# Performance work log

Hardware: AMD Instinct MI355X
Metric: run time of the kernel (lower is better)

Reference implementation:

```python
import jax, jax.numpy as jnp
import numpy as np

N, C_IN, C_OUT = 16384, 512, 1024

def setup_inputs() -> dict:
    key = jax.random.key(0)
    k1, k2 = jax.random.split(key)
    x = jax.random.normal(k1, (N, C_IN), dtype=jnp.float32)
    mean = jax.random.normal(k2, (C_OUT, C_IN), dtype=jnp.float32)
    return {"x": x, "mean": mean}

def reference(x, mean):
    # out[n, o] = 1 / sqrt(sum_c (x[n,c] - mean[o,c])^2)
    x_sq = jnp.sum(x * x, axis=-1, keepdims=True)            # [N, 1]
    m_sq = jnp.sum(mean * mean, axis=-1)                     # [O]
    cross = jnp.einsum('nc,oc->no', x, mean)                 # [N, O] GEMM
    d2 = x_sq - 2.0 * cross + m_sq[None, :]                  # [N, O]
    return jax.lax.rsqrt(d2)
```

## Files before the change

kernel.cpp:

```cpp
#include <hip/hip_runtime.h>
#include <hip/hip_bf16.h>
#include <stdint.h>

#define N_ROWS 16384
#define O_ROWS 1024
#define K_DIM  512

typedef __bf16 bf16x8 __attribute__((ext_vector_type(8)));
typedef float  f32x4  __attribute__((ext_vector_type(4)));

__device__ __forceinline__ ushort f2bfu(float f) {
    __bf16 h = (__bf16)f;
    return __builtin_bit_cast(ushort, h);
}

#define BAR_LGKM()  do {                                        \
    asm volatile("s_waitcnt lgkmcnt(0)" ::: "memory");          \
    __builtin_amdgcn_s_barrier();                               \
} while (0)

__global__ __launch_bounds__(512) void quadra_kernel(
    const float* __restrict__ x, const float* __restrict__ mean,
    float* __restrict__ out)
{
    __shared__ ushort sA[256 * 64];
    __shared__ ushort sB[128 * 64];

    const int bid  = blockIdx.x;
    const int t    = (bid & 7) * 64 + (bid >> 3);
    const int brow = (t >> 3) * 256;
    const int bcol = (t & 7) * 128;

    const int tid  = threadIdx.x;
    const int lane = tid & 63;
    const int wid  = tid >> 6;
    const int wr = wid >> 1, wc = wid & 1;

    f32x4 acc[4][4] = {};

    const int r0 = tid >> 3;
    const int q  = tid & 7;

    const float* gA = x    + (size_t)(brow + r0) * K_DIM + q * 8;
    const float* gB = mean + (size_t)(bcol + r0) * K_DIM + q * 8;

    float asq[4] = {0.f, 0.f, 0.f, 0.f};
    float bsq[2] = {0.f, 0.f};

    const int hi = lane >> 4, cl = lane & 15;

    #pragma unroll 1
    for (int kt = 0; kt < 8; ++kt) {
        #pragma unroll
        for (int i = 0; i < 4; ++i) {
            const float* p = gA + (size_t)(i * 64) * K_DIM + kt * 64;
            f32x4 v0 = *(const f32x4*)(p);
            f32x4 v1 = *(const f32x4*)(p + 4);

            asq[i] += v0[0]*v0[0] + v0[1]*v0[1] + v0[2]*v0[2] + v0[3]*v0[3]
                    + v1[0]*v1[0] + v1[1]*v1[1] + v1[2]*v1[2] + v1[3]*v1[3];

            bf16x8 cv;
            cv[0] = (__bf16)v0[0]; cv[1] = (__bf16)v0[1];
            cv[2] = (__bf16)v0[2]; cv[3] = (__bf16)v0[3];
            cv[4] = (__bf16)v1[0]; cv[5] = (__bf16)v1[1];
            cv[6] = (__bf16)v1[2]; cv[7] = (__bf16)v1[3];

            const int row = r0 + i * 64;
            const int wb  = (q * 16) ^ ((row & 7) << 4);
            *(bf16x8*)(sA + row * 64 + (wb >> 1)) = cv;
        }
        #pragma unroll
        for (int i = 0; i < 2; ++i) {
            const float* p = gB + (size_t)(i * 64) * K_DIM + kt * 64;
            f32x4 v0 = *(const f32x4*)(p);
            f32x4 v1 = *(const f32x4*)(p + 4);

            bsq[i] += v0[0]*v0[0] + v0[1]*v0[1] + v0[2]*v0[2] + v0[3]*v0[3]
                    + v1[0]*v1[0] + v1[1]*v1[1] + v1[2]*v1[2] + v1[3]*v1[3];

            bf16x8 cv;
            cv[0] = (__bf16)(v0[0] * -2.0f); cv[1] = (__bf16)(v0[1] * -2.0f);
            cv[2] = (__bf16)(v0[2] * -2.0f); cv[3] = (__bf16)(v0[3] * -2.0f);
            cv[4] = (__bf16)(v1[0] * -2.0f); cv[5] = (__bf16)(v1[1] * -2.0f);
            cv[6] = (__bf16)(v1[2] * -2.0f); cv[7] = (__bf16)(v1[3] * -2.0f);

            const int row = r0 + i * 64;
            const int wb  = (q * 16) ^ ((row & 7) << 4);
            *(bf16x8*)(sB + row * 64 + (wb >> 1)) = cv;
        }

        BAR_LGKM();

        #pragma unroll
        for (int ks = 0; ks < 2; ++ks) {
            bf16x8 a[4], b[4];
            #pragma unroll
            for (int m = 0; m < 4; ++m) {
                const int row = wr*64 + m*16 + cl;
                const int rb  = (ks*64 + hi*16) ^ ((row & 7) << 4);
                a[m] = *(const bf16x8*)(sA + row * 64 + (rb >> 1));
            }
            #pragma unroll
            for (int n = 0; n < 4; ++n) {
                const int row = wc*64 + n*16 + cl;
                const int rb  = (ks*64 + hi*16) ^ ((row & 7) << 4);
                b[n] = *(const bf16x8*)(sB + row * 64 + (rb >> 1));
            }
            #pragma unroll
            for (int m = 0; m < 4; ++m)
                #pragma unroll
                for (int n = 0; n < 4; ++n)
                    acc[m][n] = __builtin_amdgcn_mfma_f32_16x16x32_bf16(
                        a[m], b[n], acc[m][n], 0, 0, 0);
        }

        BAR_LGKM();
    }

    ushort* sAe = sA;
    ushort* sBe = sA + 256 * 32;
    #pragma unroll
    for (int i = 0; i < 4; ++i) {
        float sa = asq[i];
        #pragma unroll
        for (int msk = 1; msk < 8; msk <<= 1) sa += __shfl_xor(sa, msk);
        uint2 aw = {0u, 0u};
        if (q == 0) aw.x = (uint32_t)f2bfu(sa) | (0x3F80u << 16);
        *(uint2*)(sAe + (r0 + i * 64) * 32 + q * 4) = aw;
    }
    #pragma unroll
    for (int i = 0; i < 2; ++i) {
        float sb = bsq[i];
        #pragma unroll
        for (int msk = 1; msk < 8; msk <<= 1) sb += __shfl_xor(sb, msk);
        uint2 bw = {0u, 0u};
        if (q == 0) bw.x = 0x3F80u | ((uint32_t)f2bfu(sb) << 16);
        *(uint2*)(sBe + (r0 + i * 64) * 32 + q * 4) = bw;
    }
    BAR_LGKM();

    {
        bf16x8 a[4], b[4];
        #pragma unroll
        for (int m = 0; m < 4; ++m)
            a[m] = *(const bf16x8*)(sAe + (wr*64 + m*16 + cl) * 32 + hi * 8);
        #pragma unroll
        for (int n = 0; n < 4; ++n)
            b[n] = *(const bf16x8*)(sBe + (wc*64 + n*16 + cl) * 32 + hi * 8);
        #pragma unroll
        for (int m = 0; m < 4; ++m)
            #pragma unroll
            for (int n = 0; n < 4; ++n)
                acc[m][n] = __builtin_amdgcn_mfma_f32_16x16x32_bf16(
                    a[m], b[n], acc[m][n], 0, 0, 0);
    }

    const int rg = lane >> 4;
    #pragma unroll
    for (int m = 0; m < 4; ++m) {
        #pragma unroll
        for (int j = 0; j < 4; ++j) {
            const int grow = brow + wr*64 + m*16 + rg*4 + j;
            float* orow = out + (size_t)grow * O_ROWS + bcol + wc*64 + cl;
            #pragma unroll
            for (int n = 0; n < 4; ++n)
                orow[n * 16] = rsqrtf(acc[m][n][j]);
        }
    }
}

extern "C" void kernel_launch(void* const* d_in, const int* in_sizes, int n_in,
                              void* d_out, int out_size, void* d_ws, size_t ws_size,
                              hipStream_t stream) {
    const float* x    = (const float*)d_in[0];
    const float* mean = (const float*)d_in[1];
    float* out = (float*)d_out;

    quadra_kernel<<<dim3((N_ROWS / 256) * (O_ROWS / 128)), 512, 0, stream>>>(
        x, mean, out);
}
```

Measured before the change: 40.59 us.

## Load A fragments directly from global into registers, stage only B in LDS

```diff
diff --git a/kernel.cpp b/kernel.cpp
--- a/kernel.cpp
+++ b/kernel.cpp
@@ -19,12 +19,14 @@
     __builtin_amdgcn_s_barrier();                               \
 } while (0)
 
-__global__ __launch_bounds__(512) void quadra_kernel(
+__global__ __launch_bounds__(256, 2) void quadra_kernel(
     const float* __restrict__ x, const float* __restrict__ mean,
     float* __restrict__ out)
 {
-    __shared__ ushort sA[256 * 64];
-    __shared__ ushort sB[128 * 64];
+    __shared__ ushort lds[12288];
+    ushort* sB  = lds;
+    ushort* sAe = lds;
+    ushort* sBe = lds + 8192;
 
     const int bid  = blockIdx.x;
     const int t    = (bid & 7) * 64 + (bid >> 3);
@@ -34,83 +36,80 @@
     const int tid  = threadIdx.x;
     const int lane = tid & 63;
     const int wid  = tid >> 6;
-    const int wr = wid >> 1, wc = wid & 1;
+    const int cl   = lane & 15, hi = lane >> 4;
 
-    f32x4 acc[4][4] = {};
+    f32x4 acc[4][8] = {};
 
-    const int r0 = tid >> 3;
-    const int q  = tid & 7;
+    const int srow = tid >> 1;
+    const int h    = tid & 1;
+    const float* gB = mean + (size_t)(bcol + srow) * K_DIM + h * 32;
 
-    const float* gA = x    + (size_t)(brow + r0) * K_DIM + q * 8;
-    const float* gB = mean + (size_t)(bcol + r0) * K_DIM + q * 8;
+    const float* gA = x + (size_t)(brow + wid * 64 + cl) * K_DIM + hi * 8;
 
     float asq[4] = {0.f, 0.f, 0.f, 0.f};
-    float bsq[2] = {0.f, 0.f};
-
-    const int hi = lane >> 4, cl = lane & 15;
+    float bsq = 0.f;
 
     #pragma unroll 1
     for (int kt = 0; kt < 8; ++kt) {
         #pragma unroll
-        for (int i = 0; i < 4; ++i) {
-            const float* p = gA + (size_t)(i * 64) * K_DIM + kt * 64;
+        for (int c = 0; c < 2; ++c) {
+            const float* p = gB + kt * 64 + c * 16;
             f32x4 v0 = *(const f32x4*)(p);
             f32x4 v1 = *(const f32x4*)(p + 4);
+            f32x4 v2 = *(const f32x4*)(p + 8);
+            f32x4 v3 = *(const f32x4*)(p + 12);
 
-            asq[i] += v0[0]*v0[0] + v0[1]*v0[1] + v0[2]*v0[2] + v0[3]*v0[3]
-                    + v1[0]*v1[0] + v1[1]*v1[1] + v1[2]*v1[2] + v1[3]*v1[3];
+            bsq += v0[0]*v0[0] + v0[1]*v0[1] + v0[2]*v0[2] + v0[3]*v0[3]
+                 + v1[0]*v1[0] + v1[1]*v1[1] + v1[2]*v1[2] + v1[3]*v1[3]
+                 + v2[0]*v2[0] + v2[1]*v2[1] + v2[2]*v2[2] + v2[3]*v2[3]
+                 + v3[0]*v3[0] + v3[1]*v3[1] + v3[2]*v3[2] + v3[3]*v3[3];
 
-            bf16x8 cv;
-            cv[0] = (__bf16)v0[0]; cv[1] = (__bf16)v0[1];
-            cv[2] = (__bf16)v0[2]; cv[3] = (__bf16)v0[3];
-            cv[4] = (__bf16)v1[0]; cv[5] = (__bf16)v1[1];
-            cv[6] = (__bf16)v1[2]; cv[7] = (__bf16)v1[3];
+            bf16x8 c0, c1;
+            c0[0] = (__bf16)(v0[0] * -2.0f); c0[1] = (__bf16)(v0[1] * -2.0f);
+            c0[2] = (__bf16)(v0[2] * -2.0f); c0[3] = (__bf16)(v0[3] * -2.0f);
+            c0[4] = (__bf16)(v1[0] * -2.0f); c0[5] = (__bf16)(v1[1] * -2.0f);
+            c0[6] = (__bf16)(v1[2] * -2.0f); c0[7] = (__bf16)(v1[3] * -2.0f);
+            c1[0] = (__bf16)(v2[0] * -2.0f); c1[1] = (__bf16)(v2[1] * -2.0f);
+            c1[2] = (__bf16)(v2[2] * -2.0f); c1[3] = (__bf16)(v2[3] * -2.0f);
+            c1[4] = (__bf16)(v3[0] * -2.0f); c1[5] = (__bf16)(v3[1] * -2.0f);
+            c1[6] = (__bf16)(v3[2] * -2.0f); c1[7] = (__bf16)(v3[3] * -2.0f);
 
-            const int row = r0 + i * 64;
-            const int wb  = (q * 16) ^ ((row & 7) << 4);
-            *(bf16x8*)(sA + row * 64 + (wb >> 1)) = cv;
-        }
-        #pragma unroll
-        for (int i = 0; i < 2; ++i) {
-            const float* p = gB + (size_t)(i * 64) * K_DIM + kt * 64;
-            f32x4 v0 = *(const f32x4*)(p);
-            f32x4 v1 = *(const f32x4*)(p + 4);
-
-            bsq[i] += v0[0]*v0[0] + v0[1]*v0[1] + v0[2]*v0[2] + v0[3]*v0[3]
-                    + v1[0]*v1[0] + v1[1]*v1[1] + v1[2]*v1[2] + v1[3]*v1[3];
-
-            bf16x8 cv;
-            cv[0] = (__bf16)(v0[0] * -2.0f); cv[1] = (__bf16)(v0[1] * -2.0f);
-            cv[2] = (__bf16)(v0[2] * -2.0f); cv[3] = (__bf16)(v0[3] * -2.0f);
-            cv[4] = (__bf16)(v1[0] * -2.0f); cv[5] = (__bf16)(v1[1] * -2.0f);
-            cv[6] = (__bf16)(v1[2] * -2.0f); cv[7] = (__bf16)(v1[3] * -2.0f);
-
-            const int row = r0 + i * 64;
-            const int wb  = (q * 16) ^ ((row & 7) << 4);
-            *(bf16x8*)(sB + row * 64 + (wb >> 1)) = cv;
+            const int b0  = h * 64 + c * 32;
+            const int swz = (srow & 7) << 4;
+            *(bf16x8*)(sB + srow * 64 + (((b0)      ^ swz) >> 1)) = c0;
+            *(bf16x8*)(sB + srow * 64 + (((b0 + 16) ^ swz) >> 1)) = c1;
         }
 
         BAR_LGKM();
 
         #pragma unroll
         for (int ks = 0; ks < 2; ++ks) {
-            bf16x8 a[4], b[4];
+            bf16x8 a[4];
             #pragma unroll
             for (int m = 0; m < 4; ++m) {
-                const int row = wr*64 + m*16 + cl;
-                const int rb  = (ks*64 + hi*16) ^ ((row & 7) << 4);
-                a[m] = *(const bf16x8*)(sA + row * 64 + (rb >> 1));
+                const float* p = gA + (size_t)(m * 16) * K_DIM + kt * 64 + ks * 32;
+                f32x4 v0 = *(const f32x4*)(p);
+                f32x4 v1 = *(const f32x4*)(p + 4);
+                asq[m] += v0[0]*v0[0] + v0[1]*v0[1] + v0[2]*v0[2] + v0[3]*v0[3]
+                        + v1[0]*v1[0] + v1[1]*v1[1] + v1[2]*v1[2] + v1[3]*v1[3];
+                bf16x8 cv;
+                cv[0] = (__bf16)v0[0]; cv[1] = (__bf16)v0[1];
+                cv[2] = (__bf16)v0[2]; cv[3] = (__bf16)v0[3];
+                cv[4] = (__bf16)v1[0]; cv[5] = (__bf16)v1[1];
+                cv[6] = (__bf16)v1[2]; cv[7] = (__bf16)v1[3];
+                a[m] = cv;
             }
+            bf16x8 b[8];
             #pragma unroll
-            for (int n = 0; n < 4; ++n) {
-                const int row = wc*64 + n*16 + cl;
-                const int rb  = (ks*64 + hi*16) ^ ((row & 7) << 4);
+            for (int n = 0; n < 8; ++n) {
+                const int row = n * 16 + cl;
+                const int rb  = (ks * 64 + hi * 16) ^ ((row & 7) << 4);
                 b[n] = *(const bf16x8*)(sB + row * 64 + (rb >> 1));
             }
             #pragma unroll
             for (int m = 0; m < 4; ++m)
                 #pragma unroll
-                for (int n = 0; n < 4; ++n)
+                for (int n = 0; n < 8; ++n)
                     acc[m][n] = __builtin_amdgcn_mfma_f32_16x16x32_bf16(
                         a[m], b[n], acc[m][n], 0, 0, 0);
         }
@@ -118,53 +117,54 @@
         BAR_LGKM();
     }
 
-    ushort* sAe = sA;
-    ushort* sBe = sA + 256 * 32;
     #pragma unroll
-    for (int i = 0; i < 4; ++i) {
-        float sa = asq[i];
+    for (int m = 0; m < 4; ++m) {
+        float sa = asq[m];
+        sa += __shfl_xor(sa, 16);
+        sa += __shfl_xor(sa, 32);
+        const int row = wid * 64 + m * 16 + cl;
+        uint4 w = {0u, 0u, 0u, 0u};
+        if (hi == 0) w.x = (uint32_t)f2bfu(sa) | (0x3F80u << 16);
+        *(uint4*)(sAe + row * 32 + hi * 8) = w;
+    }
+    {
+        float sb = bsq;
+        sb += __shfl_xor(sb, 1);
         #pragma unroll
-        for (int msk = 1; msk < 8; msk <<= 1) sa += __shfl_xor(sa, msk);
-        uint2 aw = {0u, 0u};
-        if (q == 0) aw.x = (uint32_t)f2bfu(sa) | (0x3F80u << 16);
-        *(uint2*)(sAe + (r0 + i * 64) * 32 + q * 4) = aw;
-    }
-    #pragma unroll
-    for (int i = 0; i < 2; ++i) {
-        float sb = bsq[i];
-        #pragma unroll
-        for (int msk = 1; msk < 8; msk <<= 1) sb += __shfl_xor(sb, msk);
-        uint2 bw = {0u, 0u};
-        if (q == 0) bw.x = 0x3F80u | ((uint32_t)f2bfu(sb) << 16);
-        *(uint2*)(sBe + (r0 + i * 64) * 32 + q * 4) = bw;
+        for (int s = 0; s < 2; ++s) {
+            uint4 w = {0u, 0u, 0u, 0u};
+            if (h == 0 && s == 0)
+                w.x = 0x3F80u | ((uint32_t)f2bfu(sb) << 16);
+            *(uint4*)(sBe + srow * 32 + h * 16 + s * 8) = w;
+        }
     }
     BAR_LGKM();
 
     {
-        bf16x8 a[4], b[4];
+        bf16x8 a[4], b[8];
         #pragma unroll
         for (int m = 0; m < 4; ++m)
-            a[m] = *(const bf16x8*)(sAe + (wr*64 + m*16 + cl) * 32 + hi * 8);
+            a[m] = *(const bf16x8*)(sAe + (wid*64 + m*16 + cl) * 32 + hi * 8);
         #pragma unroll
-        for (int n = 0; n < 4; ++n)
-            b[n] = *(const bf16x8*)(sBe + (wc*64 + n*16 + cl) * 32 + hi * 8);
+        for (int n = 0; n < 8; ++n)
+            b[n] = *(const bf16x8*)(sBe + (n*16 + cl) * 32 + hi * 8);
         #pragma unroll
         for (int m = 0; m < 4; ++m)
             #pragma unroll
-            for (int n = 0; n < 4; ++n)
+            for (int n = 0; n < 8; ++n)
                 acc[m][n] = __builtin_amdgcn_mfma_f32_16x16x32_bf16(
                     a[m], b[n], acc[m][n], 0, 0, 0);
     }
 
-    const int rg = lane >> 4;
+    const int rg = hi;
     #pragma unroll
     for (int m = 0; m < 4; ++m) {
         #pragma unroll
         for (int j = 0; j < 4; ++j) {
-            const int grow = brow + wr*64 + m*16 + rg*4 + j;
-            float* orow = out + (size_t)grow * O_ROWS + bcol + wc*64 + cl;
+            const int grow = brow + wid*64 + m*16 + rg*4 + j;
+            float* orow = out + (size_t)grow * O_ROWS + bcol + cl;
             #pragma unroll
-            for (int n = 0; n < 4; ++n)
+            for (int n = 0; n < 8; ++n)
                 orow[n * 16] = rsqrtf(acc[m][n][j]);
         }
     }
@@ -177,6 +177,6 @@
     const float* mean = (const float*)d_in[1];
     float* out = (float*)d_out;
 
-    quadra_kernel<<<dim3((N_ROWS / 256) * (O_ROWS / 128)), 512, 0, stream>>>(
+    quadra_kernel<<<dim3((N_ROWS / 256) * (O_ROWS / 128)), 256, 0, stream>>>(
         x, mean, out);
 }
```

Result: slower. 61.09 us (+50.5%).

## Double-buffer shared tiles and prefetch next K-slice during MFMA

Applied to the files above, without the earlier changes.

```diff
diff --git a/kernel.cpp b/kernel.cpp
--- a/kernel.cpp
+++ b/kernel.cpp
@@ -6,6 +6,7 @@
 #define O_ROWS 1024
 #define K_DIM  512
 
+typedef __bf16 bf16x4 __attribute__((ext_vector_type(4)));
 typedef __bf16 bf16x8 __attribute__((ext_vector_type(8)));
 typedef float  f32x4  __attribute__((ext_vector_type(4)));
 
@@ -23,8 +24,8 @@
     const float* __restrict__ x, const float* __restrict__ mean,
     float* __restrict__ out)
 {
-    __shared__ ushort sA[256 * 64];
-    __shared__ ushort sB[128 * 64];
+    __shared__ ushort sA[2][128 * 64];
+    __shared__ ushort sB[2][64 * 64];
 
     const int bid  = blockIdx.x;
     const int t    = (bid & 7) * 64 + (bid >> 3);
@@ -35,91 +36,127 @@
     const int lane = tid & 63;
     const int wid  = tid >> 6;
     const int wr = wid >> 1, wc = wid & 1;
+    const int cl = lane & 15, hi = lane >> 4;
 
     f32x4 acc[4][4] = {};
 
     const int r0 = tid >> 3;
     const int q  = tid & 7;
 
-    const float* gA = x    + (size_t)(brow + r0) * K_DIM + q * 8;
-    const float* gB = mean + (size_t)(bcol + r0) * K_DIM + q * 8;
+    const float* gA = x    + (size_t)(brow + r0) * K_DIM + q * 4;
+    const float* gB = mean + (size_t)(bcol + r0) * K_DIM + q * 4;
 
     float asq[4] = {0.f, 0.f, 0.f, 0.f};
     float bsq[2] = {0.f, 0.f};
 
-    const int hi = lane >> 4, cl = lane & 15;
+    f32x4 pa[4], pb[2];
+
+    #pragma unroll
+    for (int i = 0; i < 4; ++i)
+        pa[i] = *(const f32x4*)(gA + (size_t)(i * 64) * K_DIM);
+    #pragma unroll
+    for (int i = 0; i < 2; ++i)
+        pb[i] = *(const f32x4*)(gB + (size_t)(i * 64) * K_DIM);
+
+    #pragma unroll
+    for (int i = 0; i < 4; ++i) {
+        f32x4 v = pa[i];
+        asq[i] += v[0]*v[0] + v[1]*v[1] + v[2]*v[2] + v[3]*v[3];
+        bf16x4 cv;
+        cv[0] = (__bf16)v[0]; cv[1] = (__bf16)v[1];
+        cv[2] = (__bf16)v[2]; cv[3] = (__bf16)v[3];
+        const int r  = r0 + i * 64;
+        const int by = ((r >> 7) * 64 + q * 8) ^ ((r & 7) << 4);
+        *(bf16x4*)(&sA[0][0] + (r & 127) * 64 + (by >> 1)) = cv;
+    }
+    #pragma unroll
+    for (int i = 0; i < 2; ++i) {
+        f32x4 v = pb[i];
+        bsq[i] += v[0]*v[0] + v[1]*v[1] + v[2]*v[2] + v[3]*v[3];
+        bf16x4 cv;
+        cv[0] = (__bf16)(v[0] * -2.0f); cv[1] = (__bf16)(v[1] * -2.0f);
+        cv[2] = (__bf16)(v[2] * -2.0f); cv[3] = (__bf16)(v[3] * -2.0f);
+        const int r  = r0 + i * 64;
+        const int by = ((r >> 6) * 64 + q * 8) ^ ((r & 7) << 4);
+        *(bf16x4*)(&sB[0][0] + (r & 63) * 64 + (by >> 1)) = cv;
+    }
+    BAR_LGKM();
 
     #pragma unroll 1
-    for (int kt = 0; kt < 8; ++kt) {
-        #pragma unroll
-        for (int i = 0; i < 4; ++i) {
-            const float* p = gA + (size_t)(i * 64) * K_DIM + kt * 64;
-            f32x4 v0 = *(const f32x4*)(p);
-            f32x4 v1 = *(const f32x4*)(p + 4);
-
-            asq[i] += v0[0]*v0[0] + v0[1]*v0[1] + v0[2]*v0[2] + v0[3]*v0[3]
-                    + v1[0]*v1[0] + v1[1]*v1[1] + v1[2]*v1[2] + v1[3]*v1[3];
-
-            bf16x8 cv;
-            cv[0] = (__bf16)v0[0]; cv[1] = (__bf16)v0[1];
-            cv[2] = (__bf16)v0[2]; cv[3] = (__bf16)v0[3];
-            cv[4] = (__bf16)v1[0]; cv[5] = (__bf16)v1[1];
-            cv[6] = (__bf16)v1[2]; cv[7] = (__bf16)v1[3];
-
-            const int row = r0 + i * 64;
-            const int wb  = (q * 16) ^ ((row & 7) << 4);
-            *(bf16x8*)(sA + row * 64 + (wb >> 1)) = cv;
-        }
-        #pragma unroll
-        for (int i = 0; i < 2; ++i) {
-            const float* p = gB + (size_t)(i * 64) * K_DIM + kt * 64;
-            f32x4 v0 = *(const f32x4*)(p);
-            f32x4 v1 = *(const f32x4*)(p + 4);
-
-            bsq[i] += v0[0]*v0[0] + v0[1]*v0[1] + v0[2]*v0[2] + v0[3]*v0[3]
-                    + v1[0]*v1[0] + v1[1]*v1[1] + v1[2]*v1[2] + v1[3]*v1[3];
-
-            bf16x8 cv;
-            cv[0] = (__bf16)(v0[0] * -2.0f); cv[1] = (__bf16)(v0[1] * -2.0f);
-            cv[2] = (__bf16)(v0[2] * -2.0f); cv[3] = (__bf16)(v0[3] * -2.0f);
-            cv[4] = (__bf16)(v1[0] * -2.0f); cv[5] = (__bf16)(v1[1] * -2.0f);
-            cv[6] = (__bf16)(v1[2] * -2.0f); cv[7] = (__bf16)(v1[3] * -2.0f);
-
-            const int row = r0 + i * 64;
-            const int wb  = (q * 16) ^ ((row & 7) << 4);
-            *(bf16x8*)(sB + row * 64 + (wb >> 1)) = cv;
-        }
+    for (int kt = 0; kt < 16; ++kt) {
+        const int cur = kt & 1;
+        ushort* bufA = &sA[cur][0];
+        ushort* bufB = &sB[cur][0];
+        ushort* nxtA = &sA[cur ^ 1][0];
+        ushort* nxtB = &sB[cur ^ 1][0];
+
+        if (kt < 15) {
+            #pragma unroll
+            for (int i = 0; i < 4; ++i)
+                pa[i] = *(const f32x4*)(gA + (size_t)(i * 64) * K_DIM + (kt + 1) * 32);
+            #pragma unroll
+            for (int i = 0; i < 2; ++i)
+                pb[i] = *(const f32x4*)(gB + (size_t)(i * 64) * K_DIM + (kt + 1) * 32);
+        }
+
+        bf16x8 a[4], b[4];
+        #pragma unroll
+        for (int m = 0; m < 4; ++m) {
+            const int rr = wr*64 + m*16 + cl;
+            const int by = ((rr >> 7) * 64 + hi * 16) ^ ((rr & 7) << 4);
+            a[m] = *(const bf16x8*)(bufA + (rr & 127) * 64 + (by >> 1));
+        }
+        #pragma unroll
+        for (int n = 0; n < 4; ++n) {
+            const int rr = wc*64 + n*16 + cl;
+            const int by = ((rr >> 6) * 64 + hi * 16) ^ ((rr & 7) << 4);
+            b[n] = *(const bf16x8*)(bufB + (rr & 63) * 64 + (by >> 1));
+        }
+
+        #pragma unroll
+        for (int m = 0; m < 2; ++m)
+            #pragma unroll
+            for (int n = 0; n < 4; ++n)
+                acc[m][n] = __builtin_amdgcn_mfma_f32_16x16x32_bf16(
+                    a[m], b[n], acc[m][n], 0, 0, 0);
+
+        if (kt < 15) {
+            #pragma unroll
+            for (int i = 0; i < 4; ++i) {
+                f32x4 v = pa[i];
+                asq[i] += v[0]*v[0] + v[1]*v[1] + v[2]*v[2] + v[3]*v[3];
+                bf16x4 cv;
+                cv[0] = (__bf16)v[0]; cv[1] = (__bf16)v[1];
+                cv[2] = (__bf16)v[2]; cv[3] = (__bf16)v[3];
+                const int r  = r0 + i * 64;
+                const int by = ((r >> 7) * 64 + q * 8) ^ ((r & 7) << 4);
+                *(bf16x4*)(nxtA + (r & 127) * 64 + (by >> 1)) = cv;
+            }
+            #pragma unroll
+            for (int i = 0; i < 2; ++i) {
+                f32x4 v = pb[i];
+                bsq[i] += v[0]*v[0] + v[1]*v[1] + v[2]*v[2] + v[3]*v[3];
+                bf16x4 cv;
+                cv[0] = (__bf16)(v[0] * -2.0f); cv[1] = (__bf16)(v[1] * -2.0f);
+                cv[2] = (__bf16)(v[2] * -2.0f); cv[3] = (__bf16)(v[3] * -2.0f);
+                const int r  = r0 + i * 64;
+                const int by = ((r >> 6) * 64 + q * 8) ^ ((r & 7) << 4);
+                *(bf16x4*)(nxtB + (r & 63) * 64 + (by >> 1)) = cv;
+            }
+        }
+
+        #pragma unroll
+        for (int m = 2; m < 4; ++m)
+            #pragma unroll
+            for (int n = 0; n < 4; ++n)
+                acc[m][n] = __builtin_amdgcn_mfma_f32_16x16x32_bf16(
+                    a[m], b[n], acc[m][n], 0, 0, 0);
 
         BAR_LGKM();
-
-        #pragma unroll
-        for (int ks = 0; ks < 2; ++ks) {
-            bf16x8 a[4], b[4];
-            #pragma unroll
-            for (int m = 0; m < 4; ++m) {
-                const int row = wr*64 + m*16 + cl;
-                const int rb  = (ks*64 + hi*16) ^ ((row & 7) << 4);
-                a[m] = *(const bf16x8*)(sA + row * 64 + (rb >> 1));
-            }
-            #pragma unroll
-            for (int n = 0; n < 4; ++n) {
-                const int row = wc*64 + n*16 + cl;
-                const int rb  = (ks*64 + hi*16) ^ ((row & 7) << 4);
-                b[n] = *(const bf16x8*)(sB + row * 64 + (rb >> 1));
-            }
-            #pragma unroll
-            for (int m = 0; m < 4; ++m)
-                #pragma unroll
-                for (int n = 0; n < 4; ++n)
-                    acc[m][n] = __builtin_amdgcn_mfma_f32_16x16x32_bf16(
-                        a[m], b[n], acc[m][n], 0, 0, 0);
-        }
-
-        BAR_LGKM();
-    }
-
-    ushort* sAe = sA;
-    ushort* sBe = sA + 256 * 32;
+    }
+
+    ushort* sAe = &sA[0][0];
+    ushort* sBe = &sA[1][0];
     #pragma unroll
     for (int i = 0; i < 4; ++i) {
         float sa = asq[i];
@@ -156,12 +193,11 @@
                     a[m], b[n], acc[m][n], 0, 0, 0);
     }
 
-    const int rg = lane >> 4;
     #pragma unroll
     for (int m = 0; m < 4; ++m) {
         #pragma unroll
         for (int j = 0; j < 4; ++j) {
-            const int grow = brow + wr*64 + m*16 + rg*4 + j;
+            const int grow = brow + wr*64 + m*16 + hi*4 + j;
             float* orow = out + (size_t)grow * O_ROWS + bcol + wc*64 + cl;
             #pragma unroll
             for (int n = 0; n < 4; ++n)
```

Result: slower. 46.05 us (+13.4%).

## Split block into producer and consumer waves with double-buffered LDS

Applied to the files above, without the earlier changes.

```diff
diff --git a/kernel.cpp b/kernel.cpp
--- a/kernel.cpp
+++ b/kernel.cpp
@@ -23,8 +23,8 @@
     const float* __restrict__ x, const float* __restrict__ mean,
     float* __restrict__ out)
 {
-    __shared__ ushort sA[256 * 64];
-    __shared__ ushort sB[128 * 64];
+    __shared__ ushort sA[2][256 * 64];
+    __shared__ ushort sB[2][128 * 64];
 
     const int bid  = blockIdx.x;
     const int t    = (bid & 7) * 64 + (bid >> 3);
@@ -34,140 +34,165 @@
     const int tid  = threadIdx.x;
     const int lane = tid & 63;
     const int wid  = tid >> 6;
-    const int wr = wid >> 1, wc = wid & 1;
-
-    f32x4 acc[4][4] = {};
-
-    const int r0 = tid >> 3;
+    const int cl = lane & 15, hi = lane >> 4;
+    const bool producer = (wid < 4);
+
+    const int r0 = (tid >> 3) & 31;
     const int q  = tid & 7;
-
+    const int rb = (tid >> 2) & 63;
+    const int qb = tid & 3;
     const float* gA = x    + (size_t)(brow + r0) * K_DIM + q * 8;
-    const float* gB = mean + (size_t)(bcol + r0) * K_DIM + q * 8;
-
-    float asq[4] = {0.f, 0.f, 0.f, 0.f};
+    const float* gB = mean + (size_t)(bcol + rb) * K_DIM + qb * 16;
+
+    const int cw = wid - 4;
+    const int cr = (cw >> 1) & 1, cc = cw & 1;
+
+    f32x4 acc[8][4] = {};
+    float asq[8] = {0,0,0,0,0,0,0,0};
     float bsq[2] = {0.f, 0.f};
 
-    const int hi = lane >> 4, cl = lane & 15;
+    #define STAGE(KT, BUF) do {                                              \
+        ushort* dA = &sA[BUF][0];                                            \
+        ushort* dB = &sB[BUF][0];                                            \
+        _Pragma("unroll")                                                    \
+        for (int i = 0; i < 8; ++i) {                                        \
+            const float* p = gA + (size_t)(i * 32) * K_DIM + (KT) * 64;      \
+            f32x4 v0 = *(const f32x4*)(p);                                   \
+            f32x4 v1 = *(const f32x4*)(p + 4);                               \
+            asq[i] += v0[0]*v0[0] + v0[1]*v0[1] + v0[2]*v0[2] + v0[3]*v0[3]  \
+                    + v1[0]*v1[0] + v1[1]*v1[1] + v1[2]*v1[2] + v1[3]*v1[3]; \
+            bf16x8 cv;                                                       \
+            cv[0] = (__bf16)v0[0]; cv[1] = (__bf16)v0[1];                    \
+            cv[2] = (__bf16)v0[2]; cv[3] = (__bf16)v0[3];                    \
+            cv[4] = (__bf16)v1[0]; cv[5] = (__bf16)v1[1];                    \
+            cv[6] = (__bf16)v1[2]; cv[7] = (__bf16)v1[3];                    \
+            const int row = r0 + i * 32;                                     \
+            const int wb  = (q * 16) ^ ((row & 7) << 4);                     \
+            *(bf16x8*)(dA + row * 64 + (wb >> 1)) = cv;                      \
+        }                                                                    \
+        _Pragma("unroll")                                                    \
+        for (int i = 0; i < 2; ++i) {                                        \
+            const float* p = gB + (size_t)(i * 64) * K_DIM + (KT) * 64;      \
+            f32x4 v0 = *(const f32x4*)(p);                                   \
+            f32x4 v1 = *(const f32x4*)(p + 4);                               \
+            f32x4 v2 = *(const f32x4*)(p + 8);                               \
+            f32x4 v3 = *(const f32x4*)(p + 12);                              \
+            bsq[i] += v0[0]*v0[0] + v0[1]*v0[1] + v0[2]*v0[2] + v0[3]*v0[3]  \
+                    + v1[0]*v1[0] + v1[1]*v1[1] + v1[2]*v1[2] + v1[3]*v1[3]  \
+                    + v2[0]*v2[0] + v2[1]*v2[1] + v2[2]*v2[2] + v2[3]*v2[3]  \
+                    + v3[0]*v3[0] + v3[1]*v3[1] + v3[2]*v3[2] + v3[3]*v3[3]; \
+            bf16x8 c0, c1;                                                   \
+            c0[0] = (__bf16)(v0[0] * -2.0f); c0[1] = (__bf16)(v0[1] * -2.0f);\
+            c0[2] = (__bf16)(v0[2] * -2.0f); c0[3] = (__bf16)(v0[3] * -2.0f);\
+            c0[4] = (__bf16)(v1[0] * -2.0f); c0[5] = (__bf16)(v1[1] * -2.0f);\
+            c0[6] = (__bf16)(v1[2] * -2.0f); c0[7] = (__bf16)(v1[3] * -2.0f);\
+            c1[0] = (__bf16)(v2[0] * -2.0f); c1[1] = (__bf16)(v2[1] * -2.0f);\
+            c1[2] = (__bf16)(v2[2] * -2.0f); c1[3] = (__bf16)(v2[3] * -2.0f);\
+            c1[4] = (__bf16)(v3[0] * -2.0f); c1[5] = (__bf16)(v3[1] * -2.0f);\
+            c1[6] = (__bf16)(v3[2] * -2.0f); c1[7] = (__bf16)(v3[3] * -2.0f);\
+            const int row = rb + i * 64;                                     \
+            const int swz = (row & 7) << 4;                                  \
+            *(bf16x8*)(dB + row * 64 + (((qb * 32)      ^ swz) >> 1)) = c0;  \
+            *(bf16x8*)(dB + row * 64 + (((qb * 32 + 16) ^ swz) >> 1)) = c1;  \
+        }                                                                    \
+    } while (0)
+
+    if (producer) STAGE(0, 0);
+    BAR_LGKM();
 
     #pragma unroll 1
     for (int kt = 0; kt < 8; ++kt) {
+        if (producer) {
+            if (kt < 7) {
+                const int nb = (kt + 1) & 1;
+                if (nb) STAGE(kt + 1, 1); else STAGE(kt + 1, 0);
+            }
+        } else {
+            const ushort* bufA = &sA[kt & 1][0];
+            const ushort* bufB = &sB[kt & 1][0];
+            #pragma unroll
+            for (int ks = 0; ks < 2; ++ks) {
+                bf16x8 a[8], b[4];
+                #pragma unroll
+                for (int m = 0; m < 8; ++m) {
+                    const int row = cr*128 + m*16 + cl;
+                    const int rbo = (ks*64 + hi*16) ^ ((row & 7) << 4);
+                    a[m] = *(const bf16x8*)(bufA + row * 64 + (rbo >> 1));
+                }
+                #pragma unroll
+                for (int n = 0; n < 4; ++n) {
+                    const int row = cc*64 + n*16 + cl;
+                    const int rbo = (ks*64 + hi*16) ^ ((row & 7) << 4);
+                    b[n] = *(const bf16x8*)(bufB + row * 64 + (rbo >> 1));
+                }
+                #pragma unroll
+                for (int m = 0; m < 8; ++m)
+                    #pragma unroll
+                    for (int n = 0; n < 4; ++n)
+                        acc[m][n] = __builtin_amdgcn_mfma_f32_16x16x32_bf16(
+                            a[m], b[n], acc[m][n], 0, 0, 0);
+            }
+        }
+        BAR_LGKM();
+    }
+
+    ushort* sAe = &sA[0][0];
+    ushort* sBe = &sB[0][0];
+    if (producer) {
         #pragma unroll
-        for (int i = 0; i < 4; ++i) {
-            const float* p = gA + (size_t)(i * 64) * K_DIM + kt * 64;
-            f32x4 v0 = *(const f32x4*)(p);
-            f32x4 v1 = *(const f32x4*)(p + 4);
-
-            asq[i] += v0[0]*v0[0] + v0[1]*v0[1] + v0[2]*v0[2] + v0[3]*v0[3]
-                    + v1[0]*v1[0] + v1[1]*v1[1] + v1[2]*v1[2] + v1[3]*v1[3];
-
-            bf16x8 cv;
-            cv[0] = (__bf16)v0[0]; cv[1] = (__bf16)v0[1];
-            cv[2] = (__bf16)v0[2]; cv[3] = (__bf16)v0[3];
-            cv[4] = (__bf16)v1[0]; cv[5] = (__bf16)v1[1];
-            cv[6] = (__bf16)v1[2]; cv[7] = (__bf16)v1[3];
-
-            const int row = r0 + i * 64;
-            const int wb  = (q * 16) ^ ((row & 7) << 4);
-            *(bf16x8*)(sA + row * 64 + (wb >> 1)) = cv;
+        for (int i = 0; i < 8; ++i) {
+            float sa = asq[i];
+            sa += __shfl_xor(sa, 1);
+            sa += __shfl_xor(sa, 2);
+            sa += __shfl_xor(sa, 4);
+            const int row = r0 + i * 32;
+            uint2 aw = {0u, 0u};
+            if (q == 0) aw.x = (uint32_t)f2bfu(sa) | (0x3F80u << 16);
+            *(uint2*)(sAe + row * 32 + q * 4) = aw;
         }
         #pragma unroll
         for (int i = 0; i < 2; ++i) {
-            const float* p = gB + (size_t)(i * 64) * K_DIM + kt * 64;
-            f32x4 v0 = *(const f32x4*)(p);
-            f32x4 v1 = *(const f32x4*)(p + 4);
-
-            bsq[i] += v0[0]*v0[0] + v0[1]*v0[1] + v0[2]*v0[2] + v0[3]*v0[3]
-                    + v1[0]*v1[0] + v1[1]*v1[1] + v1[2]*v1[2] + v1[3]*v1[3];
-
-            bf16x8 cv;
-            cv[0] = (__bf16)(v0[0] * -2.0f); cv[1] = (__bf16)(v0[1] * -2.0f);
-            cv[2] = (__bf16)(v0[2] * -2.0f); cv[3] = (__bf16)(v0[3] * -2.0f);
-            cv[4] = (__bf16)(v1[0] * -2.0f); cv[5] = (__bf16)(v1[1] * -2.0f);
-            cv[6] = (__bf16)(v1[2] * -2.0f); cv[7] = (__bf16)(v1[3] * -2.0f);
-
-            const int row = r0 + i * 64;
-            const int wb  = (q * 16) ^ ((row & 7) << 4);
-            *(bf16x8*)(sB + row * 64 + (wb >> 1)) = cv;
-        }
-
-        BAR_LGKM();
-
-        #pragma unroll
-        for (int ks = 0; ks < 2; ++ks) {
-            bf16x8 a[4], b[4];
-            #pragma unroll
-            for (int m = 0; m < 4; ++m) {
-                const int row = wr*64 + m*16 + cl;
-                const int rb  = (ks*64 + hi*16) ^ ((row & 7) << 4);
-                a[m] = *(const bf16x8*)(sA + row * 64 + (rb >> 1));
-            }
-            #pragma unroll
-            for (int n = 0; n < 4; ++n) {
-                const int row = wc*64 + n*16 + cl;
-                const int rb  = (ks*64 + hi*16) ^ ((row & 7) << 4);
-                b[n] = *(const bf16x8*)(sB + row * 64 + (rb >> 1));
-            }
-            #pragma unroll
-            for (int m = 0; m < 4; ++m)
+            float sb = bsq[i];
+            sb += __shfl_xor(sb, 1);
+            sb += __shfl_xor(sb, 2);
+            const int row = rb + i * 64;
+            uint4 bw = {0u, 0u, 0u, 0u};
+            if (qb == 0) bw.x = 0x3F80u | ((uint32_t)f2bfu(sb) << 16);
+            *(uint4*)(sBe + row * 32 + qb * 8) = bw;
+        }
+    }
+    BAR_LGKM();
+
+    if (!producer) {
+        {
+            bf16x8 a[8], b[4];
+            #pragma unroll
+            for (int m = 0; m < 8; ++m)
+                a[m] = *(const bf16x8*)(sAe + (cr*128 + m*16 + cl) * 32 + hi * 8);
+            #pragma unroll
+            for (int n = 0; n < 4; ++n)
+                b[n] = *(const bf16x8*)(sBe + (cc*64 + n*16 + cl) * 32 + hi * 8);
+            #pragma unroll
+            for (int m = 0; m < 8; ++m)
                 #pragma unroll
                 for (int n = 0; n < 4; ++n)
                     acc[m][n] = __builtin_amdgcn_mfma_f32_16x16x32_bf16(
                         a[m], b[n], acc[m][n], 0, 0, 0);
         }
 
-        BAR_LGKM();
+        #pragma unroll
+        for (int m = 0; m < 8; ++m) {
+            #pragma unroll
+            for (int j = 0; j < 4; ++j) {
+                const int grow = brow + cr*128 + m*16 + hi*4 + j;
+                float* orow = out + (size_t)grow * O_ROWS + bcol + cc*64 + cl;
+                #pragma unroll
+                for (int n = 0; n < 4; ++n)
+                    orow[n * 16] = rsqrtf(acc[m][n][j]);
+            }
+        }
     }
-
-    ushort* sAe = sA;
-    ushort* sBe = sA + 256 * 32;
-    #pragma unroll
-    for (int i = 0; i < 4; ++i) {
-        float sa = asq[i];
-        #pragma unroll
-        for (int msk = 1; msk < 8; msk <<= 1) sa += __shfl_xor(sa, msk);
-        uint2 aw = {0u, 0u};
-        if (q == 0) aw.x = (uint32_t)f2bfu(sa) | (0x3F80u << 16);
-        *(uint2*)(sAe + (r0 + i * 64) * 32 + q * 4) = aw;
-    }
-    #pragma unroll
-    for (int i = 0; i < 2; ++i) {
-        float sb = bsq[i];
-        #pragma unroll
-        for (int msk = 1; msk < 8; msk <<= 1) sb += __shfl_xor(sb, msk);
-        uint2 bw = {0u, 0u};
-        if (q == 0) bw.x = 0x3F80u | ((uint32_t)f2bfu(sb) << 16);
-        *(uint2*)(sBe + (r0 + i * 64) * 32 + q * 4) = bw;
-    }
-    BAR_LGKM();
-
-    {
-        bf16x8 a[4], b[4];
-        #pragma unroll
-        for (int m = 0; m < 4; ++m)
-            a[m] = *(const bf16x8*)(sAe + (wr*64 + m*16 + cl) * 32 + hi * 8);
-        #pragma unroll
-        for (int n = 0; n < 4; ++n)
-            b[n] = *(const bf16x8*)(sBe + (wc*64 + n*16 + cl) * 32 + hi * 8);
-        #pragma unroll
-        for (int m = 0; m < 4; ++m)
-            #pragma unroll
-            for (int n = 0; n < 4; ++n)
-                acc[m][n] = __builtin_amdgcn_mfma_f32_16x16x32_bf16(
-                    a[m], b[n], acc[m][n], 0, 0, 0);
-    }
-
-    const int rg = lane >> 4;
-    #pragma unroll
-    for (int m = 0; m < 4; ++m) {
-        #pragma unroll
-        for (int j = 0; j < 4; ++j) {
-            const int grow = brow + wr*64 + m*16 + rg*4 + j;
-            float* orow = out + (size_t)grow * O_ROWS + bcol + wc*64 + cl;
-            #pragma unroll
-            for (int n = 0; n < 4; ++n)
-                orow[n * 16] = rsqrtf(acc[m][n][j]);
-        }
-    }
+    #undef STAGE
 }
 
 extern "C" void kernel_launch(void* const* d_in, const int* in_sizes, int n_in,
```

Result: slower. 61.74 us (+52.1%).
